# Performance work log

Hardware: AMD Instinct MI355X
Metric: run time of the kernel (lower is better)

## Reference

```python
import jax, jax.numpy as jnp
from jax import lax
import numpy as np

N_REPEAT = 200  # the Python loop count in the original module


def setup_inputs() -> dict:
    key = jax.random.key(0)
    k_x, k_w1, k_b1, k_w2, k_b2 = jax.random.split(key, 5)
    x = jax.random.normal(k_x, (4, 3, 70, 70), dtype=jnp.float32)
    # conv1: Conv2d(3, 64, 7) -> OIHW weight [64, 3, 7, 7]
    W1 = jax.random.normal(k_w1, (64, 3, 7, 7), dtype=jnp.float32) * (1.0 / np.sqrt(3 * 7 * 7))
    b1 = jax.random.normal(k_b1, (64,), dtype=jnp.float32) * 0.01
    # conv2: Conv2d(64, 64, 1) -> channel-mix matrix [64, 64] (O, I)
    W2 = jax.random.normal(k_w2, (64, 64), dtype=jnp.float32) * (1.0 / np.sqrt(64))
    b2 = jax.random.normal(k_b2, (64,), dtype=jnp.float32) * 0.01
    return {"x": x, "W1": W1, "b1": b1, "W2": W2, "b2": b2}


def reference(x, W1, b1, W2, b2):
    # 7x7 VALID conv: [4,3,70,70] -> [4,64,64,64]
    h = lax.conv_general_dilated(
        x, W1, window_strides=(1, 1), padding="VALID",
        dimension_numbers=("NCHW", "OIHW", "NCHW"),
    ) + b1[None, :, None, None]

    # 200 repeated identical 1x1 convs == repeated channel GEMM with shared W2, b2
    def step(h, _):
        h = jnp.einsum("oc,bchw->bohw", W2, h) + b2[None, :, None, None]
        return h, None

    h, _ = lax.scan(step, h, None, length=N_REPEAT)
    return h
```

## Files before the change

### kernel.cpp

```cpp
#include <hip/hip_runtime.h>


#define S72 72

__device__ __forceinline__ void mm64(const float* AT, const float* B,
                                     float* D, float* DT, int r0, int c0)
{
  float acc[4][4];
#pragma unroll
  for (int i = 0; i < 4; ++i)
#pragma unroll
    for (int j = 0; j < 4; ++j) acc[i][j] = 0.f;

#pragma unroll 8
  for (int k = 0; k < 64; ++k) {
    const float4 a  = *(const float4*)(AT + k * S72 + r0);
    const float4 bv = *(const float4*)(B  + k * S72 + c0);
    const float av[4] = {a.x, a.y, a.z, a.w};
    const float bb[4] = {bv.x, bv.y, bv.z, bv.w};
#pragma unroll
    for (int i = 0; i < 4; ++i)
#pragma unroll
      for (int j = 0; j < 4; ++j) acc[i][j] += av[i] * bb[j];
  }
#pragma unroll
  for (int i = 0; i < 4; ++i)
    *(float4*)(D + (r0 + i) * S72 + c0) =
        make_float4(acc[i][0], acc[i][1], acc[i][2], acc[i][3]);
#pragma unroll
  for (int j = 0; j < 4; ++j)
    *(float4*)(DT + (c0 + j) * S72 + r0) =
        make_float4(acc[0][j], acc[1][j], acc[2][j], acc[3][j]);
}

__global__ __launch_bounds__(256) void chain_kernel(
    const float* __restrict__ W2g, const float* __restrict__ b2g,
    const float* __restrict__ b1g, float* __restrict__ ws)
{
  __shared__ float Wm[64 * S72];
  __shared__ float buf0[64 * S72], buf0T[64 * S72];
  __shared__ float buf1[64 * S72], buf1T[64 * S72];
  __shared__ float vv[64], tv[64], b2s[64];

  const int t = threadIdx.x;
  for (int i = t; i < 4096; i += 256) {
    const int r = i >> 6, c = i & 63;
    const float w = W2g[i];
    Wm[r * S72 + c]    = w;
    buf0[r * S72 + c]  = w;
    buf0T[c * S72 + r] = w;
  }
  if (t < 64) { const float b = b2g[t]; vv[t] = b; b2s[t] = b; }
  __syncthreads();

  float *P = buf0, *PT = buf0T, *T = buf1, *TT = buf1T;
  const int r0 = (t >> 4) << 2;
  const int c0 = (t & 15) << 2;

#pragma unroll
  for (int s = 0; s < 7; ++s) {
    if (t < 64) {
      float a = 0.f;
#pragma unroll 8
      for (int k = 0; k < 64; ++k) a += PT[k * S72 + t] * vv[k];
      tv[t] = vv[t] + a;
    }
    __syncthreads();
    mm64(PT, P, T, TT, r0, c0);
    __syncthreads();
    if (t < 64) vv[t] = tv[t];
    { float* x = P; P = T; T = x; x = PT; PT = TT; TT = x; }
    __syncthreads();

    if (s == 0 || s == 3) {
      if (t < 64) {
        float a = 0.f;
#pragma unroll 8
        for (int k = 0; k < 64; ++k) a += PT[k * S72 + t] * b2s[k];
        tv[t] = vv[t] + a;
      }
      __syncthreads();
      mm64(PT, Wm, T, TT, r0, c0);
      __syncthreads();
      if (t < 64) vv[t] = tv[t];
      { float* x = P; P = T; T = x; x = PT; PT = TT; TT = x; }
      __syncthreads();
    }
  }

  for (int i = t; i < 4096; i += 256)
    ws[i] = P[(i >> 6) * S72 + (i & 63)];
  if (t < 64) {
    float a = 0.f;
#pragma unroll 8
    for (int k = 0; k < 64; ++k) a += PT[k * S72 + t] * b1g[k];
    ws[4096 + t] = a + vv[t];
  }
}

__global__ __launch_bounds__(192) void w1eff_kernel(
    const float* __restrict__ W1g, float* __restrict__ ws)
{
  const int o = blockIdx.x;
  const int j = threadIdx.x;
  if (j >= 147) return;
  const float* Prow = ws + o * 64;
  float a = 0.f;
#pragma unroll 8
  for (int c = 0; c < 64; ++c) a += Prow[c] * W1g[c * 147 + j];
  ws[4160 + o * 147 + j] = a;
}

__global__ __launch_bounds__(256) void conv_kernel(
    const float* __restrict__ xg, const float* __restrict__ ws,
    float* __restrict__ out)
{
  __shared__ float xs[1470];
  __shared__ float Wls[9408];
  __shared__ float bs[64];

  const int t = threadIdx.x;
  const int bid = blockIdx.x;
  const int b = bid >> 7, y = (bid >> 1) & 63, xh = bid & 1;

  for (int i = t; i < 1470; i += 256) {
    const int c = i / 490, rem = i - c * 490;
    const int ky = rem / 70, col = rem - ky * 70;
    xs[i] = xg[((b * 3 + c) * 70 + (y + ky)) * 70 + col];
  }
  const float4* wg4 = (const float4*)(ws + 4160);
  float4* wl4 = (float4*)Wls;
  for (int i = t; i < 2352; i += 256) wl4[i] = wg4[i];
  if (t < 64) bs[t] = ws[4096 + t];
  __syncthreads();

  const int o = t & 63, pg = t >> 6;
  const int x0 = xh * 32 + pg * 8;

  float acc[8];
  const float bv = bs[o];
#pragma unroll
  for (int j = 0; j < 8; ++j) acc[j] = bv;

  for (int c = 0; c < 3; ++c) {
#pragma unroll
    for (int ky = 0; ky < 7; ++ky) {
      const float* xrow = &xs[(c * 7 + ky) * 70 + x0];
      float xw[14];
#pragma unroll
      for (int u = 0; u < 14; ++u) xw[u] = xrow[u];
      const float* wrow = &Wls[o * 147 + c * 49 + ky * 7];
#pragma unroll
      for (int kx = 0; kx < 7; ++kx) {
        const float w = wrow[kx];
#pragma unroll
        for (int j = 0; j < 8; ++j) acc[j] += w * xw[kx + j];
      }
    }
  }

  float* op = out + (((b * 64 + o) * 64 + y) * 64) + x0;
  *(float4*)op       = make_float4(acc[0], acc[1], acc[2], acc[3]);
  *(float4*)(op + 4) = make_float4(acc[4], acc[5], acc[6], acc[7]);
}

extern "C" void kernel_launch(void* const* d_in, const int* in_sizes, int n_in,
                              void* d_out, int out_size, void* d_ws, size_t ws_size,
                              hipStream_t stream) {
  const float* x  = (const float*)d_in[0];
  const float* W1 = (const float*)d_in[1];
  const float* b1 = (const float*)d_in[2];
  const float* W2 = (const float*)d_in[3];
  const float* b2 = (const float*)d_in[4];
  float* out = (float*)d_out;
  float* ws  = (float*)d_ws;

  chain_kernel<<<1, 256, 0, stream>>>(W2, b2, b1, ws);
  w1eff_kernel<<<64, 192, 0, stream>>>(W1, ws);
  conv_kernel<<<512, 256, 0, stream>>>(x, ws, out);
}
```

Baseline: 51.66 us.

## Compute W2 power chain with split-bf16 MFMA across 16 waves

The single-block chain kernel that raises W2 to the 200th power by repeated squaring now uses bf16 MFMA instructions with a hi/lo split (three MFMAs per k-step) to approximate fp32 accuracy. It runs 1024 threads, one 16x16 output tile per wave, with XOR-swizzled LDS layouts, and the W2 fragments are held in registers. Each step now needs one barrier instead of three. The aim is to shorten the serial latency of this one-block kernel. The cost is lower precision from dropping the lo*lo term, which is compounded over many squarings.

```diff
diff --git a/kernel.cpp b/kernel.cpp
--- a/kernel.cpp
+++ b/kernel.cpp
@@ -1,100 +1,142 @@
 #include <hip/hip_runtime.h>
 
 
-#define S72 72
-
-__device__ __forceinline__ void mm64(const float* AT, const float* B,
-                                     float* D, float* DT, int r0, int c0)
-{
-  float acc[4][4];
-#pragma unroll
-  for (int i = 0; i < 4; ++i)
-#pragma unroll
-    for (int j = 0; j < 4; ++j) acc[i][j] = 0.f;
-
+typedef __attribute__((ext_vector_type(8))) short bf16x8;
+typedef __attribute__((ext_vector_type(4))) short bf16x4;
+typedef __attribute__((ext_vector_type(4))) float f32x4;
+
+__device__ __forceinline__ short f2bf(float x) {
+  unsigned u = __float_as_uint(x);
+  return (short)((u + 0x7fffu + ((u >> 16) & 1u)) >> 16);
+}
+__device__ __forceinline__ float bf2f(short h) {
+  return __uint_as_float(((unsigned)(unsigned short)h) << 16);
+}
+
+__device__ __forceinline__ bf16x8 ldfrag(const short* buf, int r, int k0) {
+  int s = (r * 64 + k0) ^ ((r & 7) << 3);
+  return *(const bf16x8*)(buf + s);
+}
+
+template <bool USEW2>
+__device__ __forceinline__ void do_mul(
+    const short* ah_, const short* al_, const short* bth, const short* btl,
+    bf16x8 w2h0, bf16x8 w2h1, bf16x8 w2l0, bf16x8 w2l1,
+    short* dh, short* dl, short* dth, short* dtl,
+    int tr, int tc, int frow, int fkb)
+{
+  f32x4 acc = {0.f, 0.f, 0.f, 0.f};
+#pragma unroll
+  for (int s = 0; s < 2; ++s) {
+    const int k0 = 32 * s + 8 * fkb;
+    bf16x8 Ah = ldfrag(ah_, 16 * tr + frow, k0);
+    bf16x8 Al = ldfrag(al_, 16 * tr + frow, k0);
+    bf16x8 Bh = USEW2 ? (s == 0 ? w2h0 : w2h1) : ldfrag(bth, 16 * tc + frow, k0);
+    bf16x8 Bl = USEW2 ? (s == 0 ? w2l0 : w2l1) : ldfrag(btl, 16 * tc + frow, k0);
+    acc = __builtin_amdgcn_mfma_f32_16x16x32_bf16(Ah, Bh, acc, 0, 0, 0);
+    acc = __builtin_amdgcn_mfma_f32_16x16x32_bf16(Ah, Bl, acc, 0, 0, 0);
+    acc = __builtin_amdgcn_mfma_f32_16x16x32_bf16(Al, Bh, acc, 0, 0, 0);
+  }
+  const int ocol = 16 * tc + frow;
+  const int orow0 = 16 * tr + fkb * 4;
+  bf16x4 h4, l4;
+#pragma unroll
+  for (int j = 0; j < 4; ++j) {
+    const float x = acc[j];
+    const short h = f2bf(x);
+    const short l = f2bf(x - bf2f(h));
+    const int r = orow0 + j;
+    dh[(r * 64 + ocol) ^ ((r & 7) << 3)] = h;
+    dl[(r * 64 + ocol) ^ ((r & 7) << 3)] = l;
+    h4[j] = h; l4[j] = l;
+  }
+  const int si = (ocol * 64 + orow0) ^ ((ocol & 7) << 3);
+  *(bf16x4*)(dth + si) = h4;
+  *(bf16x4*)(dtl + si) = l4;
+}
+
+__device__ __forceinline__ float vupd(const short* pth, const short* ptl,
+                                      float u, float vin, int lane) {
+  float a = 0.f;
 #pragma unroll 8
   for (int k = 0; k < 64; ++k) {
-    const float4 a  = *(const float4*)(AT + k * S72 + r0);
-    const float4 bv = *(const float4*)(B  + k * S72 + c0);
-    const float av[4] = {a.x, a.y, a.z, a.w};
-    const float bb[4] = {bv.x, bv.y, bv.z, bv.w};
-#pragma unroll
-    for (int i = 0; i < 4; ++i)
-#pragma unroll
-      for (int j = 0; j < 4; ++j) acc[i][j] += av[i] * bb[j];
-  }
-#pragma unroll
-  for (int i = 0; i < 4; ++i)
-    *(float4*)(D + (r0 + i) * S72 + c0) =
-        make_float4(acc[i][0], acc[i][1], acc[i][2], acc[i][3]);
-#pragma unroll
-  for (int j = 0; j < 4; ++j)
-    *(float4*)(DT + (c0 + j) * S72 + r0) =
-        make_float4(acc[0][j], acc[1][j], acc[2][j], acc[3][j]);
-}
-
-__global__ __launch_bounds__(256) void chain_kernel(
+    const int si = (k * 64 + lane) ^ ((k & 7) << 3);
+    a += (bf2f(pth[si]) + bf2f(ptl[si])) * __shfl(u, k, 64);
+  }
+  return vin + a;
+}
+
+__global__ __launch_bounds__(1024) void chain_kernel(
     const float* __restrict__ W2g, const float* __restrict__ b2g,
     const float* __restrict__ b1g, float* __restrict__ ws)
 {
-  __shared__ float Wm[64 * S72];
-  __shared__ float buf0[64 * S72], buf0T[64 * S72];
-  __shared__ float buf1[64 * S72], buf1T[64 * S72];
-  __shared__ float vv[64], tv[64], b2s[64];
+  __shared__ __align__(16) short B0h[4096], B0l[4096], B0Th[4096], B0Tl[4096];
+  __shared__ __align__(16) short B1h[4096], B1l[4096], B1Th[4096], B1Tl[4096];
 
   const int t = threadIdx.x;
-  for (int i = t; i < 4096; i += 256) {
+  const int wid = t >> 6, lane = t & 63;
+  const int tr = wid >> 2, tc = wid & 3;
+  const int frow = lane & 15, fkb = lane >> 4;
+
+  for (int i = t; i < 4096; i += 1024) {
     const int r = i >> 6, c = i & 63;
     const float w = W2g[i];
-    Wm[r * S72 + c]    = w;
-    buf0[r * S72 + c]  = w;
-    buf0T[c * S72 + r] = w;
-  }
-  if (t < 64) { const float b = b2g[t]; vv[t] = b; b2s[t] = b; }
+    const short h = f2bf(w);
+    const short l = f2bf(w - bf2f(h));
+    B0h[(r * 64 + c) ^ ((r & 7) << 3)] = h;
+    B0l[(r * 64 + c) ^ ((r & 7) << 3)] = l;
+    B0Th[(c * 64 + r) ^ ((c & 7) << 3)] = h;
+    B0Tl[(c * 64 + r) ^ ((c & 7) << 3)] = l;
+  }
+
+  bf16x8 w2h0, w2h1, w2l0, w2l1;
+#pragma unroll
+  for (int j = 0; j < 8; ++j) {
+    {
+      const float w = W2g[(8 * fkb + j) * 64 + 16 * tc + frow];
+      const short h = f2bf(w);
+      w2h0[j] = h; w2l0[j] = f2bf(w - bf2f(h));
+    }
+    {
+      const float w = W2g[(32 + 8 * fkb + j) * 64 + 16 * tc + frow];
+      const short h = f2bf(w);
+      w2h1[j] = h; w2l1[j] = f2bf(w - bf2f(h));
+    }
+  }
+
+  float vc = 0.f, b2r = 0.f;
+  if (wid == 0) { b2r = b2g[lane]; vc = b2r; }
+
+  short *ph = B0h, *pl = B0l, *pth = B0Th, *ptl = B0Tl;
+  short *dh = B1h, *dl = B1l, *dth = B1Th, *dtl = B1Tl;
+
+#pragma unroll
+  for (int s7 = 0; s7 < 7; ++s7) {
+    __syncthreads();
+    if (wid == 0) vc = vupd(pth, ptl, vc, vc, lane);
+    do_mul<false>(ph, pl, pth, ptl, w2h0, w2h1, w2l0, w2l1,
+                  dh, dl, dth, dtl, tr, tc, frow, fkb);
+    { short* x; x=ph; ph=dh; dh=x; x=pl; pl=dl; dl=x;
+      x=pth; pth=dth; dth=x; x=ptl; ptl=dtl; dtl=x; }
+    if (s7 == 0 || s7 == 3) {
+      __syncthreads();
+      if (wid == 0) vc = vupd(pth, ptl, b2r, vc, lane);
+      do_mul<true>(ph, pl, nullptr, nullptr, w2h0, w2h1, w2l0, w2l1,
+                   dh, dl, dth, dtl, tr, tc, frow, fkb);
+      { short* x; x=ph; ph=dh; dh=x; x=pl; pl=dl; dl=x;
+        x=pth; pth=dth; dth=x; x=ptl; ptl=dtl; dtl=x; }
+    }
+  }
   __syncthreads();
 
-  float *P = buf0, *PT = buf0T, *T = buf1, *TT = buf1T;
-  const int r0 = (t >> 4) << 2;
-  const int c0 = (t & 15) << 2;
-
-#pragma unroll
-  for (int s = 0; s < 7; ++s) {
-    if (t < 64) {
-      float a = 0.f;
-#pragma unroll 8
-      for (int k = 0; k < 64; ++k) a += PT[k * S72 + t] * vv[k];
-      tv[t] = vv[t] + a;
-    }
-    __syncthreads();
-    mm64(PT, P, T, TT, r0, c0);
-    __syncthreads();
-    if (t < 64) vv[t] = tv[t];
-    { float* x = P; P = T; T = x; x = PT; PT = TT; TT = x; }
-    __syncthreads();
-
-    if (s == 0 || s == 3) {
-      if (t < 64) {
-        float a = 0.f;
-#pragma unroll 8
-        for (int k = 0; k < 64; ++k) a += PT[k * S72 + t] * b2s[k];
-        tv[t] = vv[t] + a;
-      }
-      __syncthreads();
-      mm64(PT, Wm, T, TT, r0, c0);
-      __syncthreads();
-      if (t < 64) vv[t] = tv[t];
-      { float* x = P; P = T; T = x; x = PT; PT = TT; TT = x; }
-      __syncthreads();
-    }
-  }
-
-  for (int i = t; i < 4096; i += 256)
-    ws[i] = P[(i >> 6) * S72 + (i & 63)];
-  if (t < 64) {
-    float a = 0.f;
-#pragma unroll 8
-    for (int k = 0; k < 64; ++k) a += PT[k * S72 + t] * b1g[k];
-    ws[4096 + t] = a + vv[t];
+  for (int i = t; i < 4096; i += 1024) {
+    const int r = i >> 6, c = i & 63;
+    const int si = (r * 64 + c) ^ ((r & 7) << 3);
+    ws[i] = bf2f(ph[si]) + bf2f(pl[si]);
+  }
+  if (wid == 0) {
+    const float b1r = b1g[lane];
+    ws[4096 + lane] = vupd(pth, ptl, b1r, vc, lane);
   }
 }
 
@@ -175,7 +217,7 @@
   float* out = (float*)d_out;
   float* ws  = (float*)d_ws;
 
-  chain_kernel<<<1, 256, 0, stream>>>(W2, b2, b1, ws);
+  chain_kernel<<<1, 1024, 0, stream>>>(W2, b2, b1, ws);
   w1eff_kernel<<<64, 192, 0, stream>>>(W1, ws);
   conv_kernel<<<512, 256, 0, stream>>>(x, ws, out);
 }
```

After: 42.43 us. 17.9% less time.
